# Kernel tuning notes

Hardware: AMD Instinct MI355X
Metric: run time of the kernel (lower is better)

Reference implementation:

```python
import jax, jax.numpy as jnp
import numpy as np

D_IN, D_HIDDEN, D_OUT, BATCH = 128, 512, 128, 65536


def setup_inputs() -> dict:
    key = jax.random.key(0)
    k_x, k_u, k_a, k_b, k_c = jax.random.split(key, 5)
    return {
        "x": jax.random.normal(k_x, (BATCH, D_HIDDEN), dtype=jnp.float32),
        "u": jax.random.normal(k_u, (BATCH, D_IN), dtype=jnp.float32),
        "a": jax.random.normal(k_a, (D_HIDDEN,), dtype=jnp.float32),
        "b": jax.random.normal(k_b, (D_IN, D_HIDDEN), dtype=jnp.float32),
        "c": jax.random.normal(k_c, (D_HIDDEN, D_OUT), dtype=jnp.float32),
    }


def reference(x, u, a, b, c):
    # Diagonal linear RNN step: new state = decay * x + u @ b, then output GEMM.
    decay = jax.nn.softmax(a)  # [d_hidden]
    x_new = x * decay[None, :] + u @ b  # [B, d_hidden]
    output = x_new @ c  # [B, d_out]
    return (x_new, output)
```

## Files before the change

kernel.cpp:

```cpp
#include <hip/hip_runtime.h>
#include <hip/hip_bf16.h>

#define BATCH 65536
#define DIN   128
#define DH    512
#define DOUT  128
#define ROWS  32

typedef __attribute__((ext_vector_type(4))) float f32x4;
typedef __attribute__((ext_vector_type(8))) short s16x8;

__device__ __forceinline__ ushort f32_to_bf16_rn(float f) {
    uint32_t u = __float_as_uint(f);
    uint32_t r = (u + 0x7FFFu + ((u >> 16) & 1u)) >> 16;
    return (ushort)r;
}
__device__ __forceinline__ float bf16_to_f32(ushort h) {
    return __uint_as_float(((uint32_t)h) << 16);
}
__device__ __forceinline__ f32x4 mfma16(s16x8 a, s16x8 b, f32x4 c) {
    return __builtin_amdgcn_mfma_f32_16x16x32_bf16(a, b, c, 0, 0, 0);
}
__device__ __forceinline__ s16x8 cvt8(f32x4 v0, f32x4 v1) {
    s16x8 r;
#pragma unroll
    for (int j = 0; j < 4; ++j) r[j] = (short)f32_to_bf16_rn(v0[j]);
#pragma unroll
    for (int j = 0; j < 4; ++j) r[4 + j] = (short)f32_to_bf16_rn(v1[j]);
    return r;
}

__global__ void prep_kernel(const float* __restrict__ a,
                            const float* __restrict__ b,
                            const float* __restrict__ c,
                            float* __restrict__ decay,
                            ushort* __restrict__ bhi,
                            ushort* __restrict__ chi)
{
    const int t = threadIdx.x;
    if (blockIdx.x == 0) {
        __shared__ float red[256];
        float v0 = a[t], v1 = a[t + 256];
        red[t] = fmaxf(v0, v1);
        __syncthreads();
        for (int s = 128; s > 0; s >>= 1) {
            if (t < s) red[t] = fmaxf(red[t], red[t + s]);
            __syncthreads();
        }
        float M = red[0];
        __syncthreads();
        float e0 = expf(v0 - M), e1 = expf(v1 - M);
        red[t] = e0 + e1;
        __syncthreads();
        for (int s = 128; s > 0; s >>= 1) {
            if (t < s) red[t] += red[t + s];
            __syncthreads();
        }
        float S = red[0];
        decay[t]       = e0 / S;
        decay[t + 256] = e1 / S;
    } else {
        const int p = (blockIdx.x - 1) * 256 + t;
        const int mtx = p >> 13;
        const int q = p & 8191;
        const int f = q >> 6;
        const int l = q & 63;
        s16x8 hi;
        if (mtx == 0) {
            const int cg = f >> 2, ks = f & 3;
            const int col = cg * 16 + (l & 15);
            const int kbase = ks * 32 + (l >> 4) * 8;
#pragma unroll
            for (int j = 0; j < 8; ++j)
                hi[j] = (short)f32_to_bf16_rn(b[(size_t)(kbase + j) * DH + col]);
            *(s16x8*)(bhi + (size_t)q * 8) = hi;
        } else {
            const int cg = f >> 4, ks = f & 15;
            const int col = cg * 16 + (l & 15);
            const int kbase = ks * 32 + (l >> 4) * 8;
#pragma unroll
            for (int j = 0; j < 8; ++j)
                hi[j] = (short)f32_to_bf16_rn(c[(size_t)(kbase + j) * DOUT + col]);
            *(s16x8*)(chi + (size_t)q * 8) = hi;
        }
    }
}

__global__ __launch_bounds__(256, 6)
void rnn_fused(const float* __restrict__ u, const float* __restrict__ x,
               const float* __restrict__ decay,
               const ushort* __restrict__ bhi, const ushort* __restrict__ chi,
               float* __restrict__ xn, float* __restrict__ out)
{
    __shared__ __align__(16) char smem[16384];
    ushort* Ah = (ushort*)smem;

    const int t = threadIdx.x;
    const int lane = t & 63, wc = t >> 6;
    const int cl = lane & 15, hk = lane >> 4;
    const int row0 = blockIdx.x * ROWS;

    {
        const int r = t >> 3;
        const int kb = (t & 7) * 2;
#pragma unroll
        for (int i = 0; i < 2; ++i) {
            const float* src = u + (size_t)(row0 + r) * DIN + (kb + i) * 8;
            f32x4 v0 = *(const f32x4*)src;
            f32x4 v1 = *(const f32x4*)(src + 4);
            const int byte = (r * 256 + (kb + i) * 16) ^ ((r & 7) << 4);
            *(s16x8*)((char*)Ah + byte) = cvt8(v0, v1);
        }
    }
    __syncthreads();

    f32x4 acc2[2][2];
#pragma unroll
    for (int mf = 0; mf < 2; ++mf)
#pragma unroll
        for (int nf = 0; nf < 2; ++nf)
            acc2[mf][nf] = (f32x4){0.f, 0.f, 0.f, 0.f};

    for (int ct = 0; ct < 8; ++ct) {
        char* Xh = smem + 8192 + (ct & 1) * 4096;

        const int col = ct * 64 + wc * 16 + cl;
        const float dvc = decay[col];
        float xv[2][4];
#pragma unroll
        for (int mf = 0; mf < 2; ++mf)
#pragma unroll
            for (int j = 0; j < 4; ++j)
                xv[mf][j] = x[(size_t)(row0 + mf * 16 + 4 * hk + j) * DH + col];

        f32x4 acc1[2];
        acc1[0] = (f32x4){0.f, 0.f, 0.f, 0.f};
        acc1[1] = (f32x4){0.f, 0.f, 0.f, 0.f};
#pragma unroll
        for (int ks = 0; ks < 4; ++ks) {
            const int ko = ks * 32 + hk * 8;
            s16x8 ah[2];
#pragma unroll
            for (int mf = 0; mf < 2; ++mf) {
                const int r = mf * 16 + cl;
                const int byte = (r * 256 + ko * 2) ^ ((r & 7) << 4);
                ah[mf] = *(const s16x8*)((const char*)Ah + byte);
            }
            const size_t fB = (size_t)((ct * 4 + wc) * 4 + ks) * 512 + lane * 8;
            s16x8 bh = *(const s16x8*)(bhi + fB);
#pragma unroll
            for (int mf = 0; mf < 2; ++mf) acc1[mf] = mfma16(ah[mf], bh, acc1[mf]);
        }

        __syncthreads();

#pragma unroll
        for (int mf = 0; mf < 2; ++mf) {
#pragma unroll
            for (int j = 0; j < 4; ++j) {
                const int rl = mf * 16 + 4 * hk + j;
                const float v = acc1[mf][j] + dvc * xv[mf][j];
                xn[(size_t)(row0 + rl) * DH + col] = v;
                const int cbyte = (rl * 128 + (wc * 16 + cl) * 2) ^ ((rl & 7) << 4);
                *(ushort*)(Xh + cbyte) = f32_to_bf16_rn(v);
            }
        }
        __syncthreads();

#pragma unroll
        for (int ks2 = 0; ks2 < 2; ++ks2) {
            const int ko = ks2 * 32 + hk * 8;
            s16x8 ah2[2];
#pragma unroll
            for (int mf = 0; mf < 2; ++mf) {
                const int r = mf * 16 + cl;
                const int byte = (r * 128 + ko * 2) ^ ((r & 7) << 4);
                ah2[mf] = *(const s16x8*)((const char*)Xh + byte);
            }
            const int ksg = ct * 2 + ks2;
#pragma unroll
            for (int nf = 0; nf < 2; ++nf) {
                const size_t fC = (size_t)((wc * 2 + nf) * 16 + ksg) * 512 + lane * 8;
                s16x8 ch = *(const s16x8*)(chi + fC);
#pragma unroll
                for (int mf = 0; mf < 2; ++mf)
                    acc2[mf][nf] = mfma16(ah2[mf], ch, acc2[mf][nf]);
            }
        }
    }

#pragma unroll
    for (int nf = 0; nf < 2; ++nf) {
        const int ocol = wc * 32 + nf * 16 + cl;
#pragma unroll
        for (int mf = 0; mf < 2; ++mf) {
#pragma unroll
            for (int j = 0; j < 4; ++j) {
                const int rl = mf * 16 + 4 * hk + j;
                out[(size_t)(row0 + rl) * DOUT + ocol] = acc2[mf][nf][j];
            }
        }
    }
}

extern "C" void kernel_launch(void* const* d_in, const int* in_sizes, int n_in,
                              void* d_out, int out_size, void* d_ws, size_t ws_size,
                              hipStream_t stream)
{
    const float* x = (const float*)d_in[0];
    const float* u = (const float*)d_in[1];
    const float* a = (const float*)d_in[2];
    const float* b = (const float*)d_in[3];
    const float* c = (const float*)d_in[4];

    float* xn  = (float*)d_out;
    float* out = xn + (size_t)BATCH * DH;

    char* ws = (char*)d_ws;
    float*  decay = (float*)ws;
    ushort* bhi = (ushort*)(ws + 4096);
    ushort* chi = bhi + 128 * 512;

    prep_kernel<<<dim3(65), dim3(256), 0, stream>>>(a, b, c, decay, bhi, chi);
    rnn_fused<<<dim3(BATCH / ROWS), dim3(256), 0, stream>>>(u, x, decay, bhi, chi, xn, out);
}
```

Measured before the change: 108.5 us.

## Give each wave its own 16-row slab to drop block-level barriers

Each block now handles 64 rows, and each wave owns 16 of them end to end, with its own LDS staging for u and for the bf16 hidden tile. All __syncthreads calls go away because no wave reads data written by another wave. In exchange every wave loads all B and C fragments itself, which raises L2/global traffic for weights. LDS use doubles and launch bounds drop to 4 blocks per CU.

```diff
diff --git a/kernel.cpp b/kernel.cpp
--- a/kernel.cpp
+++ b/kernel.cpp
@@ -5,7 +5,7 @@
 #define DIN   128
 #define DH    512
 #define DOUT  128
-#define ROWS  32
+#define ROWS  64
 
 typedef __attribute__((ext_vector_type(4))) float f32x4;
 typedef __attribute__((ext_vector_type(8))) short s16x8;
@@ -86,120 +86,102 @@
     }
 }
 
-__global__ __launch_bounds__(256, 6)
+__global__ __launch_bounds__(256, 4)
 void rnn_fused(const float* __restrict__ u, const float* __restrict__ x,
                const float* __restrict__ decay,
                const ushort* __restrict__ bhi, const ushort* __restrict__ chi,
                float* __restrict__ xn, float* __restrict__ out)
 {
-    __shared__ __align__(16) char smem[16384];
-    ushort* Ah = (ushort*)smem;
+    __shared__ __align__(16) char smem[32768];
 
     const int t = threadIdx.x;
-    const int lane = t & 63, wc = t >> 6;
+    const int lane = t & 63, w = t >> 6;
     const int cl = lane & 15, hk = lane >> 4;
     const int row0 = blockIdx.x * ROWS;
+    const int wrow = row0 + w * 16;
+
+    char* Aw = smem + w * 4096;
+    char* Xb = smem + 16384 + w * 4096;
 
     {
-        const int r = t >> 3;
-        const int kb = (t & 7) * 2;
-#pragma unroll
-        for (int i = 0; i < 2; ++i) {
-            const float* src = u + (size_t)(row0 + r) * DIN + (kb + i) * 8;
-            f32x4 v0 = *(const f32x4*)src;
-            f32x4 v1 = *(const f32x4*)(src + 4);
-            const int byte = (r * 256 + (kb + i) * 16) ^ ((r & 7) << 4);
-            *(s16x8*)((char*)Ah + byte) = cvt8(v0, v1);
-        }
-    }
-    __syncthreads();
-
-    f32x4 acc2[2][2];
-#pragma unroll
-    for (int mf = 0; mf < 2; ++mf)
-#pragma unroll
-        for (int nf = 0; nf < 2; ++nf)
-            acc2[mf][nf] = (f32x4){0.f, 0.f, 0.f, 0.f};
+        const int lr = lane >> 2;
+        const int cb = (lane & 3) * 32;
+        const float* src = u + (size_t)(wrow + lr) * DIN + cb;
+#pragma unroll
+        for (int i = 0; i < 4; ++i) {
+            f32x4 v0 = *(const f32x4*)(src + i * 8);
+            f32x4 v1 = *(const f32x4*)(src + i * 8 + 4);
+            const int byte = (lr * 256 + (cb + i * 8) * 2) ^ ((lr & 7) << 4);
+            *(s16x8*)(Aw + byte) = cvt8(v0, v1);
+        }
+    }
+
+    f32x4 acc2[8];
+#pragma unroll
+    for (int nf2 = 0; nf2 < 8; ++nf2) acc2[nf2] = (f32x4){0.f, 0.f, 0.f, 0.f};
 
     for (int ct = 0; ct < 8; ++ct) {
-        char* Xh = smem + 8192 + (ct & 1) * 4096;
-
-        const int col = ct * 64 + wc * 16 + cl;
-        const float dvc = decay[col];
-        float xv[2][4];
-#pragma unroll
-        for (int mf = 0; mf < 2; ++mf)
+        char* Xh = Xb + (ct & 1) * 2048;
+
+        float xv[4][4], dv[4];
+#pragma unroll
+        for (int nf = 0; nf < 4; ++nf) {
+            const int col = ct * 64 + nf * 16 + cl;
+            dv[nf] = decay[col];
 #pragma unroll
             for (int j = 0; j < 4; ++j)
-                xv[mf][j] = x[(size_t)(row0 + mf * 16 + 4 * hk + j) * DH + col];
-
-        f32x4 acc1[2];
-        acc1[0] = (f32x4){0.f, 0.f, 0.f, 0.f};
-        acc1[1] = (f32x4){0.f, 0.f, 0.f, 0.f};
+                xv[nf][j] = x[(size_t)(wrow + 4 * hk + j) * DH + col];
+        }
+
+        f32x4 acc1[4];
+#pragma unroll
+        for (int nf = 0; nf < 4; ++nf) acc1[nf] = (f32x4){0.f, 0.f, 0.f, 0.f};
 #pragma unroll
         for (int ks = 0; ks < 4; ++ks) {
             const int ko = ks * 32 + hk * 8;
-            s16x8 ah[2];
-#pragma unroll
-            for (int mf = 0; mf < 2; ++mf) {
-                const int r = mf * 16 + cl;
-                const int byte = (r * 256 + ko * 2) ^ ((r & 7) << 4);
-                ah[mf] = *(const s16x8*)((const char*)Ah + byte);
+            const int abyte = (cl * 256 + ko * 2) ^ ((cl & 7) << 4);
+            s16x8 ah = *(const s16x8*)(Aw + abyte);
+#pragma unroll
+            for (int nf = 0; nf < 4; ++nf) {
+                const size_t fB = (size_t)((ct * 4 + nf) * 4 + ks) * 512 + lane * 8;
+                s16x8 bh = *(const s16x8*)(bhi + fB);
+                acc1[nf] = mfma16(ah, bh, acc1[nf]);
             }
-            const size_t fB = (size_t)((ct * 4 + wc) * 4 + ks) * 512 + lane * 8;
-            s16x8 bh = *(const s16x8*)(bhi + fB);
-#pragma unroll
-            for (int mf = 0; mf < 2; ++mf) acc1[mf] = mfma16(ah[mf], bh, acc1[mf]);
-        }
-
-        __syncthreads();
-
-#pragma unroll
-        for (int mf = 0; mf < 2; ++mf) {
+        }
+
+#pragma unroll
+        for (int nf = 0; nf < 4; ++nf) {
+            const int col = ct * 64 + nf * 16 + cl;
 #pragma unroll
             for (int j = 0; j < 4; ++j) {
-                const int rl = mf * 16 + 4 * hk + j;
-                const float v = acc1[mf][j] + dvc * xv[mf][j];
-                xn[(size_t)(row0 + rl) * DH + col] = v;
-                const int cbyte = (rl * 128 + (wc * 16 + cl) * 2) ^ ((rl & 7) << 4);
-                *(ushort*)(Xh + cbyte) = f32_to_bf16_rn(v);
+                const int lr = 4 * hk + j;
+                const float v = acc1[nf][j] + dv[nf] * xv[nf][j];
+                xn[(size_t)(wrow + lr) * DH + col] = v;
+                const int cb = (lr * 128 + (nf * 16 + cl) * 2) ^ ((lr & 7) << 4);
+                *(ushort*)(Xh + cb) = f32_to_bf16_rn(v);
             }
         }
-        __syncthreads();
 
 #pragma unroll
         for (int ks2 = 0; ks2 < 2; ++ks2) {
-            const int ko = ks2 * 32 + hk * 8;
-            s16x8 ah2[2];
-#pragma unroll
-            for (int mf = 0; mf < 2; ++mf) {
-                const int r = mf * 16 + cl;
-                const int byte = (r * 128 + ko * 2) ^ ((r & 7) << 4);
-                ah2[mf] = *(const s16x8*)((const char*)Xh + byte);
+            const int xbyte = (cl * 128 + (ks2 * 32 + hk * 8) * 2) ^ ((cl & 7) << 4);
+            s16x8 xh = *(const s16x8*)(Xh + xbyte);
+            const int ksg = ct * 2 + ks2;
+#pragma unroll
+            for (int nf2 = 0; nf2 < 8; ++nf2) {
+                const size_t fC = (size_t)(nf2 * 16 + ksg) * 512 + lane * 8;
+                s16x8 ch = *(const s16x8*)(chi + fC);
+                acc2[nf2] = mfma16(xh, ch, acc2[nf2]);
             }
-            const int ksg = ct * 2 + ks2;
-#pragma unroll
-            for (int nf = 0; nf < 2; ++nf) {
-                const size_t fC = (size_t)((wc * 2 + nf) * 16 + ksg) * 512 + lane * 8;
-                s16x8 ch = *(const s16x8*)(chi + fC);
-#pragma unroll
-                for (int mf = 0; mf < 2; ++mf)
-                    acc2[mf][nf] = mfma16(ah2[mf], ch, acc2[mf][nf]);
-            }
-        }
-    }
-
-#pragma unroll
-    for (int nf = 0; nf < 2; ++nf) {
-        const int ocol = wc * 32 + nf * 16 + cl;
-#pragma unroll
-        for (int mf = 0; mf < 2; ++mf) {
-#pragma unroll
-            for (int j = 0; j < 4; ++j) {
-                const int rl = mf * 16 + 4 * hk + j;
-                out[(size_t)(row0 + rl) * DOUT + ocol] = acc2[mf][nf][j];
-            }
-        }
+        }
+    }
+
+#pragma unroll
+    for (int nf2 = 0; nf2 < 8; ++nf2) {
+        const int ocol = nf2 * 16 + cl;
+#pragma unroll
+        for (int j = 0; j < 4; ++j)
+            out[(size_t)(wrow + 4 * hk + j) * DOUT + ocol] = acc2[nf2][j];
     }
 }
 
```

After: 148.2 us. +36.7%, slower.

## Stage GEMM tile through LDS for vectorized x loads and xn stores, prefetch x

Applied to the files above, without the earlier changes.

The first GEMM's accumulator fragments now go through a padded fp32 LDS tile, so each thread handles 8 contiguous columns of one row. The x loads, the decay loads, the x_new stores and the bf16 staging writes all become 16-byte vector accesses instead of scattered 4-byte ones in MFMA layout. The next column tile's x values are prefetched into registers one iteration ahead. The Xh buffer is now single-buffered, so an extra LDS round trip is added and shared memory grows to about 20.9 KB, which may reduce occupancy.

```diff
diff --git a/kernel.cpp b/kernel.cpp
--- a/kernel.cpp
+++ b/kernel.cpp
@@ -92,8 +92,10 @@
                const ushort* __restrict__ bhi, const ushort* __restrict__ chi,
                float* __restrict__ xn, float* __restrict__ out)
 {
-    __shared__ __align__(16) char smem[16384];
+    __shared__ __align__(16) char smem[20896];
     ushort* Ah = (ushort*)smem;
+    float*  T  = (float*)(smem + 8192);
+    char*   Xh = smem + 16896;
 
     const int t = threadIdx.x;
     const int lane = t & 63, wc = t >> 6;
@@ -112,6 +114,15 @@
             *(s16x8*)((char*)Ah + byte) = cvt8(v0, v1);
         }
     }
+
+    const int r2 = t >> 3;
+    const int c0 = (t & 7) * 8;
+    const float* xrow = x + (size_t)(row0 + r2) * DH + c0;
+
+    f32x4 xc0 = *(const f32x4*)xrow;
+    f32x4 xc1 = *(const f32x4*)(xrow + 4);
+    f32x4 xr0, xr1;
+
     __syncthreads();
 
     f32x4 acc2[2][2];
@@ -122,17 +133,6 @@
             acc2[mf][nf] = (f32x4){0.f, 0.f, 0.f, 0.f};
 
     for (int ct = 0; ct < 8; ++ct) {
-        char* Xh = smem + 8192 + (ct & 1) * 4096;
-
-        const int col = ct * 64 + wc * 16 + cl;
-        const float dvc = decay[col];
-        float xv[2][4];
-#pragma unroll
-        for (int mf = 0; mf < 2; ++mf)
-#pragma unroll
-            for (int j = 0; j < 4; ++j)
-                xv[mf][j] = x[(size_t)(row0 + mf * 16 + 4 * hk + j) * DH + col];
-
         f32x4 acc1[2];
         acc1[0] = (f32x4){0.f, 0.f, 0.f, 0.f};
         acc1[1] = (f32x4){0.f, 0.f, 0.f, 0.f};
@@ -152,19 +152,33 @@
             for (int mf = 0; mf < 2; ++mf) acc1[mf] = mfma16(ah[mf], bh, acc1[mf]);
         }
 
-        __syncthreads();
-
-#pragma unroll
-        for (int mf = 0; mf < 2; ++mf) {
-#pragma unroll
-            for (int j = 0; j < 4; ++j) {
-                const int rl = mf * 16 + 4 * hk + j;
-                const float v = acc1[mf][j] + dvc * xv[mf][j];
-                xn[(size_t)(row0 + rl) * DH + col] = v;
-                const int cbyte = (rl * 128 + (wc * 16 + cl) * 2) ^ ((rl & 7) << 4);
-                *(ushort*)(Xh + cbyte) = f32_to_bf16_rn(v);
-            }
-        }
+#pragma unroll
+        for (int mf = 0; mf < 2; ++mf)
+#pragma unroll
+            for (int j = 0; j < 4; ++j)
+                T[(mf * 16 + 4 * hk + j) * 68 + wc * 16 + cl] = acc1[mf][j];
+
+        if (ct < 7) {
+            xr0 = *(const f32x4*)(xrow + (ct + 1) * 64);
+            xr1 = *(const f32x4*)(xrow + (ct + 1) * 64 + 4);
+        }
+
+        __syncthreads();
+
+        {
+            const f32x4 t0 = *(const f32x4*)&T[r2 * 68 + c0];
+            const f32x4 t1 = *(const f32x4*)&T[r2 * 68 + c0 + 4];
+            const f32x4 d0 = *(const f32x4*)&decay[ct * 64 + c0];
+            const f32x4 d1 = *(const f32x4*)&decay[ct * 64 + c0 + 4];
+            const f32x4 v0 = t0 + d0 * xc0;
+            const f32x4 v1 = t1 + d1 * xc1;
+            float* dst = xn + (size_t)(row0 + r2) * DH + ct * 64 + c0;
+            *(f32x4*)dst       = v0;
+            *(f32x4*)(dst + 4) = v1;
+            const int xbyte = (r2 * 128 + c0 * 2) ^ ((r2 & 7) << 4);
+            *(s16x8*)(Xh + xbyte) = cvt8(v0, v1);
+        }
+
         __syncthreads();
 
 #pragma unroll
@@ -187,6 +201,9 @@
                     acc2[mf][nf] = mfma16(ah2[mf], ch, acc2[mf][nf]);
             }
         }
+
+        xc0 = xr0;
+        xc1 = xr1;
     }
 
 #pragma unroll
```

Result: slower. 117.0 us (+7.8%).

## Software-pipeline B, C, decay and x loads across column tiles

Applied to the files above, without the earlier changes.

Register-prefetches the next column tile's B fragments, decay value and x values during the current tile, and hoists the C fragment loads to the start of each tile. One of the two per-iteration barriers is removed, which is safe because the Xh buffer is double-buffered. Occupancy is lowered from 6 to 4 waves per SIMD to make room for the extra registers. The aim is to hide global-load latency behind the MFMA work, at the cost of fewer resident waves to hide latency in other places.

```diff
diff --git a/kernel.cpp b/kernel.cpp
--- a/kernel.cpp
+++ b/kernel.cpp
@@ -86,7 +86,7 @@
     }
 }
 
-__global__ __launch_bounds__(256, 6)
+__global__ __launch_bounds__(256, 4)
 void rnn_fused(const float* __restrict__ u, const float* __restrict__ x,
                const float* __restrict__ decay,
                const ushort* __restrict__ bhi, const ushort* __restrict__ chi,
@@ -112,6 +112,20 @@
             *(s16x8*)((char*)Ah + byte) = cvt8(v0, v1);
         }
     }
+
+    s16x8 bF[4], bFn[4];
+#pragma unroll
+    for (int ks = 0; ks < 4; ++ks)
+        bF[ks] = *(const s16x8*)(bhi + (size_t)(wc * 4 + ks) * 512 + lane * 8);
+
+    float xv[2][4], xvn[2][4], dvc, dvn;
+    dvc = decay[wc * 16 + cl];
+#pragma unroll
+    for (int mf = 0; mf < 2; ++mf)
+#pragma unroll
+        for (int j = 0; j < 4; ++j)
+            xv[mf][j] = x[(size_t)(row0 + mf * 16 + 4 * hk + j) * DH + wc * 16 + cl];
+
     __syncthreads();
 
     f32x4 acc2[2][2];
@@ -124,14 +138,13 @@
     for (int ct = 0; ct < 8; ++ct) {
         char* Xh = smem + 8192 + (ct & 1) * 4096;
 
-        const int col = ct * 64 + wc * 16 + cl;
-        const float dvc = decay[col];
-        float xv[2][4];
-#pragma unroll
-        for (int mf = 0; mf < 2; ++mf)
-#pragma unroll
-            for (int j = 0; j < 4; ++j)
-                xv[mf][j] = x[(size_t)(row0 + mf * 16 + 4 * hk + j) * DH + col];
+        s16x8 cF[2][2];
+#pragma unroll
+        for (int ks2 = 0; ks2 < 2; ++ks2)
+#pragma unroll
+            for (int nf = 0; nf < 2; ++nf)
+                cF[ks2][nf] = *(const s16x8*)(chi +
+                    (size_t)((wc * 2 + nf) * 16 + ct * 2 + ks2) * 512 + lane * 8);
 
         f32x4 acc1[2];
         acc1[0] = (f32x4){0.f, 0.f, 0.f, 0.f};
@@ -146,25 +159,39 @@
                 const int byte = (r * 256 + ko * 2) ^ ((r & 7) << 4);
                 ah[mf] = *(const s16x8*)((const char*)Ah + byte);
             }
-            const size_t fB = (size_t)((ct * 4 + wc) * 4 + ks) * 512 + lane * 8;
-            s16x8 bh = *(const s16x8*)(bhi + fB);
-#pragma unroll
-            for (int mf = 0; mf < 2; ++mf) acc1[mf] = mfma16(ah[mf], bh, acc1[mf]);
-        }
-
-        __syncthreads();
-
-#pragma unroll
-        for (int mf = 0; mf < 2; ++mf) {
-#pragma unroll
-            for (int j = 0; j < 4; ++j) {
-                const int rl = mf * 16 + 4 * hk + j;
-                const float v = acc1[mf][j] + dvc * xv[mf][j];
-                xn[(size_t)(row0 + rl) * DH + col] = v;
-                const int cbyte = (rl * 128 + (wc * 16 + cl) * 2) ^ ((rl & 7) << 4);
-                *(ushort*)(Xh + cbyte) = f32_to_bf16_rn(v);
-            }
-        }
+#pragma unroll
+            for (int mf = 0; mf < 2; ++mf) acc1[mf] = mfma16(ah[mf], bF[ks], acc1[mf]);
+        }
+
+        if (ct < 7) {
+#pragma unroll
+            for (int ks = 0; ks < 4; ++ks)
+                bFn[ks] = *(const s16x8*)(bhi +
+                    (size_t)(((ct + 1) * 4 + wc) * 4 + ks) * 512 + lane * 8);
+            const int ncol = (ct + 1) * 64 + wc * 16 + cl;
+            dvn = decay[ncol];
+#pragma unroll
+            for (int mf = 0; mf < 2; ++mf)
+#pragma unroll
+                for (int j = 0; j < 4; ++j)
+                    xvn[mf][j] = x[(size_t)(row0 + mf * 16 + 4 * hk + j) * DH + ncol];
+        }
+
+        {
+            const int col = ct * 64 + wc * 16 + cl;
+#pragma unroll
+            for (int mf = 0; mf < 2; ++mf) {
+#pragma unroll
+                for (int j = 0; j < 4; ++j) {
+                    const int rl = mf * 16 + 4 * hk + j;
+                    const float v = acc1[mf][j] + dvc * xv[mf][j];
+                    xn[(size_t)(row0 + rl) * DH + col] = v;
+                    const int cbyte = (rl * 128 + (wc * 16 + cl) * 2) ^ ((rl & 7) << 4);
+                    *(ushort*)(Xh + cbyte) = f32_to_bf16_rn(v);
+                }
+            }
+        }
+
         __syncthreads();
 
 #pragma unroll
@@ -177,16 +204,20 @@
                 const int byte = (r * 128 + ko * 2) ^ ((r & 7) << 4);
                 ah2[mf] = *(const s16x8*)((const char*)Xh + byte);
             }
-            const int ksg = ct * 2 + ks2;
-#pragma unroll
-            for (int nf = 0; nf < 2; ++nf) {
-                const size_t fC = (size_t)((wc * 2 + nf) * 16 + ksg) * 512 + lane * 8;
-                s16x8 ch = *(const s16x8*)(chi + fC);
+#pragma unroll
+            for (int nf = 0; nf < 2; ++nf)
 #pragma unroll
                 for (int mf = 0; mf < 2; ++mf)
-                    acc2[mf][nf] = mfma16(ah2[mf], ch, acc2[mf][nf]);
-            }
-        }
+                    acc2[mf][nf] = mfma16(ah2[mf], cF[ks2][nf], acc2[mf][nf]);
+        }
+
+#pragma unroll
+        for (int ks = 0; ks < 4; ++ks) bF[ks] = bFn[ks];
+        dvc = dvn;
+#pragma unroll
+        for (int mf = 0; mf < 2; ++mf)
+#pragma unroll
+            for (int j = 0; j < 4; ++j) xv[mf][j] = xvn[mf][j];
     }
 
 #pragma unroll
```

New measurement: 103.3 us. 4.7% less time.
